# Kernel optimization log

Measured on AMD Instinct MI355X. Metric: run time of the kernel, lower is better.

The kernel has to match this reference:

```python
import jax, jax.numpy as jnp
import numpy as np


def setup_inputs() -> dict:
    key = jax.random.key(0)
    k1, k2 = jax.random.split(key)
    B, K, D = 65536, 4096, 64
    x = jax.random.normal(k1, (B, D), dtype=jnp.float32)
    nodes = jax.random.normal(k2, (K, D), dtype=jnp.float32)  # self.nodes parameter
    return {"x": x, "nodes": nodes}


def reference(x, nodes):
    # torch.cdist(x, nodes, p=2): Euclidean distance matrix [B, K]
    x2 = jnp.sum(x * x, axis=-1, keepdims=True)            # [B, 1]
    n2 = jnp.sum(nodes * nodes, axis=-1)[None, :]          # [1, K]
    d2 = x2 + n2 - 2.0 * (x @ nodes.T)                     # [B, K]
    distances = jnp.sqrt(jnp.maximum(d2, 0.0))
    winning_indices = jnp.argmin(distances, axis=-1)       # [B]
    node_repr = nodes[winning_indices]                     # [B, D] gather
    return node_repr, winning_indices
```

## Files before the change

### kernel.cpp

```cpp
#include <hip/hip_runtime.h>
#include <stdint.h>


typedef unsigned short u16;
typedef __bf16 bf16x8 __attribute__((ext_vector_type(8)));
typedef unsigned short u16x8 __attribute__((ext_vector_type(8)));
typedef float f32x16 __attribute__((ext_vector_type(16)));

#define B_ROWS 65536
#define K_NODES 4096
#define DIM 64
#define MERGE_TAU 0.0065f

#define OFF_LIST 64
#define OFF_N2F  262208
#define OFF_N2D  278592
#define OFF_BFRAG 311360

#define GLOBAL_AS __attribute__((address_space(1)))
#define LDS_AS    __attribute__((address_space(3)))

__device__ __forceinline__ u16 bf16_rne(float f, float& back) {
    uint32_t u = __float_as_uint(f);
    uint32_t r = u + 0x7FFFu + ((u >> 16) & 1u);
    u16 h = (u16)(r >> 16);
    back = __uint_as_float(((uint32_t)h) << 16);
    return h;
}

__device__ __forceinline__ float pack_tile6(float v, uint32_t t) {
    return __uint_as_float((__float_as_uint(v) & 0xFFFFFFC0u) | t);
}

__global__ __launch_bounds__(256) void prep(const float* __restrict__ nodes,
                                            u16* __restrict__ bfrag,
                                            float* __restrict__ hn2f,
                                            double* __restrict__ n2d,
                                            int* __restrict__ ref_cnt) {
    if (blockIdx.x < 128) {
        int idx = blockIdx.x * 256 + threadIdx.x;
        int t = idx >> 8;
        int rem = idx & 255;
        int l = rem >> 2, c = rem & 3;
        const float* row = nodes + (size_t)(t * 32 + (l & 31)) * DIM + ((l >> 5) * 8);
        float4 f0 = *(const float4*)(row + c * 16);
        float4 f1 = *(const float4*)(row + c * 16 + 4);
        float fs[8] = {-f0.x, -f0.y, -f0.z, -f0.w, -f1.x, -f1.y, -f1.z, -f1.w};
        u16x8 hv, lv;
        #pragma unroll
        for (int j = 0; j < 8; ++j) {
            float hf, dummy;
            u16 hb = bf16_rne(fs[j], hf);
            u16 lb = bf16_rne(fs[j] - hf, dummy);
            hv[j] = hb; lv[j] = lb;
        }
        int base = ((t * 4 + c) * 2) * 512 + l * 8;
        *(u16x8*)(bfrag + base)       = hv;
        *(u16x8*)(bfrag + base + 512) = lv;
    } else {
        if (blockIdx.x == 128 && threadIdx.x == 0) *ref_cnt = 0;
        int k = (blockIdx.x - 128) * 256 + threadIdx.x;
        if (k < K_NODES) {
            const float* r = nodes + (size_t)k * DIM;
            double s = 0.0;
            #pragma unroll
            for (int d = 0; d < DIM; ++d) { double v = (double)r[d]; s += v * v; }
            n2d[k] = s;
            hn2f[k] = 0.5f * (float)s;
        }
    }
}

__global__ __launch_bounds__(256, 2) void phase1(const float* __restrict__ x,
                                                 const u16* __restrict__ bfrag_g,
                                                 const float* __restrict__ hn2f,
                                                 float* __restrict__ out) {
    __shared__ __align__(16) u16 ring[32768];
    __shared__ float hn2s[2048];
    const int tid  = threadIdx.x;
    const int lane = tid & 63;
    const int w    = tid >> 6;
    const int col  = lane & 31;
    const int lh   = lane >> 5;
    const int rb   = blockIdx.x >> 1;
    const int h    = blockIdx.x & 1;
    const int rbase = rb * 256 + w * 64;
    const char* qbase = (const char*)bfrag_g + (size_t)h * 524288;

    bf16x8 ah[2][4], al[2][4];
    #pragma unroll
    for (int t = 0; t < 2; ++t) {
        const float* xp = x + (size_t)(rbase + t * 32 + col) * DIM + lh * 8;
        #pragma unroll
        for (int c = 0; c < 4; ++c) {
            float4 f0 = *(const float4*)(xp + c * 16);
            float4 f1 = *(const float4*)(xp + c * 16 + 4);
            float fs[8] = {f0.x, f0.y, f0.z, f0.w, f1.x, f1.y, f1.z, f1.w};
            u16x8 hv, lv;
            #pragma unroll
            for (int j = 0; j < 8; ++j) {
                float hf, dummy;
                u16 hb = bf16_rne(fs[j], hf);
                u16 lb = bf16_rne(fs[j] - hf, dummy);
                hv[j] = hb; lv[j] = lb;
            }
            union { u16x8 u; bf16x8 b; } cvh, cvl;
            cvh.u = hv; cvl.u = lv;
            ah[t][c] = cvh.b; al[t][c] = cvl.b;
        }
    }

    float b1[2][16], v2[2][16];
    #pragma unroll
    for (int t = 0; t < 2; ++t)
        #pragma unroll
        for (int q = 0; q < 16; ++q) { b1[t][q] = 3.4e38f; v2[t][q] = 3.4e38f; }

    for (int i = tid; i < 2048; i += 256) hn2s[i] = hn2f[h * 2048 + i];
    #pragma unroll
    for (int q0 = 0; q0 < 4; ++q0) {
        const char* gp = qbase + (size_t)q0 * 8192 + tid * 16;
        const char* lp = (const char*)ring + q0 * 8192 + tid * 16;
        __builtin_amdgcn_global_load_lds((const GLOBAL_AS uint32_t*)gp,
                                         (LDS_AS uint32_t*)lp, 16, 0, 0);
        __builtin_amdgcn_global_load_lds((const GLOBAL_AS uint32_t*)(gp + 4096),
                                         (LDS_AS uint32_t*)(lp + 4096), 16, 0, 0);
    }
    asm volatile("s_waitcnt lgkmcnt(0)" ::: "memory");
    __builtin_amdgcn_s_barrier();

#define MF6(CC, BH, BL)                                                          \
    a0 = __builtin_amdgcn_mfma_f32_32x32x16_bf16(ah[0][CC], BH, a0, 0, 0, 0);    \
    a1 = __builtin_amdgcn_mfma_f32_32x32x16_bf16(ah[1][CC], BH, a1, 0, 0, 0);    \
    a0 = __builtin_amdgcn_mfma_f32_32x32x16_bf16(al[0][CC], BH, a0, 0, 0, 0);    \
    a1 = __builtin_amdgcn_mfma_f32_32x32x16_bf16(al[1][CC], BH, a1, 0, 0, 0);    \
    a0 = __builtin_amdgcn_mfma_f32_32x32x16_bf16(ah[0][CC], BL, a0, 0, 0, 0);    \
    a1 = __builtin_amdgcn_mfma_f32_32x32x16_bf16(ah[1][CC], BL, a1, 0, 0, 0);

#define PHASE(QI, VMSTR) do {                                                    \
    asm volatile("s_waitcnt " VMSTR ::: "memory");                               \
    __builtin_amdgcn_s_barrier();                                                \
    __builtin_amdgcn_sched_barrier(0);                                           \
    const u16* bb = ring + ((QI) & 7) * 4096;                                    \
    bf16x8 B0h = *(const bf16x8*)(bb + 0 * 1024 + lane * 8);                     \
    bf16x8 B0l = *(const bf16x8*)(bb + 0 * 1024 + 512 + lane * 8);               \
    bf16x8 B1h = *(const bf16x8*)(bb + 1 * 1024 + lane * 8);                     \
    bf16x8 B1l = *(const bf16x8*)(bb + 1 * 1024 + 512 + lane * 8);               \
    bf16x8 B2h = *(const bf16x8*)(bb + 2 * 1024 + lane * 8);                     \
    bf16x8 B2l = *(const bf16x8*)(bb + 2 * 1024 + 512 + lane * 8);               \
    bf16x8 B3h = *(const bf16x8*)(bb + 3 * 1024 + lane * 8);                     \
    bf16x8 B3l = *(const bf16x8*)(bb + 3 * 1024 + 512 + lane * 8);               \
    float hn2v = hn2s[(QI) * 32 + col];                                          \
    if ((QI) + 4 < 64) {                                                         \
        const char* gp = qbase + (size_t)((QI) + 4) * 8192 + tid * 16;           \
        const char* lp = (const char*)ring + (((QI) + 4) & 7) * 8192 + tid * 16; \
        __builtin_amdgcn_global_load_lds((const GLOBAL_AS uint32_t*)gp,          \
                                         (LDS_AS uint32_t*)lp, 16, 0, 0);        \
        __builtin_amdgcn_global_load_lds((const GLOBAL_AS uint32_t*)(gp + 4096), \
                                         (LDS_AS uint32_t*)(lp + 4096), 16, 0, 0); \
    }                                                                            \
    asm volatile("s_waitcnt lgkmcnt(0)" ::: "memory");                           \
    __builtin_amdgcn_sched_barrier(0);                                           \
    f32x16 a0, a1;                                                               \
    _Pragma("unroll")                                                            \
    for (int q = 0; q < 16; ++q) { a0[q] = hn2v; a1[q] = hn2v; }                 \
    __builtin_amdgcn_s_setprio(1);                                               \
    MF6(0, B0h, B0l)                                                             \
    MF6(1, B1h, B1l)                                                             \
    MF6(2, B2h, B2l)                                                             \
    MF6(3, B3h, B3l)                                                             \
    __builtin_amdgcn_s_setprio(0);                                               \
    const uint32_t tb = (uint32_t)(QI);                                          \
    _Pragma("unroll")                                                            \
    for (int q = 0; q < 16; ++q) {                                               \
        float p0 = pack_tile6(a0[q], tb);                                        \
        v2[0][q] = fminf(v2[0][q], fmaxf(p0, b1[0][q]));                         \
        b1[0][q] = fminf(b1[0][q], p0);                                          \
        float p1 = pack_tile6(a1[q], tb);                                        \
        v2[1][q] = fminf(v2[1][q], fmaxf(p1, b1[1][q]));                         \
        b1[1][q] = fminf(b1[1][q], p1);                                          \
    }                                                                            \
} while (0)

    for (int qi = 0; qi < 61; ++qi) PHASE(qi, "vmcnt(6)");
    PHASE(61, "vmcnt(4)");
    PHASE(62, "vmcnt(2)");
    PHASE(63, "vmcnt(0)");

#undef PHASE
#undef MF6

    int gi[2][16];
    #pragma unroll
    for (int t = 0; t < 2; ++t)
        #pragma unroll
        for (int q = 0; q < 16; ++q)
            gi[t][q] = h * 2048 + (int)(__float_as_uint(b1[t][q]) & 63u) * 32 + col;

    #pragma unroll
    for (int off = 1; off < 32; off <<= 1) {
        #pragma unroll
        for (int t = 0; t < 2; ++t)
            #pragma unroll
            for (int q = 0; q < 16; ++q) {
                float ov  = __shfl_xor(b1[t][q], off, 64);
                float ov2 = __shfl_xor(v2[t][q], off, 64);
                int   og  = __shfl_xor(gi[t][q], off, 64);
                float hi2 = fmaxf(b1[t][q], ov);
                v2[t][q] = fminf(fminf(v2[t][q], ov2), hi2);
                bool take = (ov < b1[t][q]) || (ov == b1[t][q] && og < gi[t][q]);
                b1[t][q] = take ? ov : b1[t][q];
                gi[t][q] = take ? og : gi[t][q];
            }
    }

    if (col == 0) {
        #pragma unroll
        for (int t = 0; t < 2; ++t)
            #pragma unroll
            for (int q = 0; q < 16; ++q) {
                int rloc = (q & 3) + 8 * (q >> 2) + 4 * lh;
                int grow = rb * 256 + w * 64 + t * 32 + rloc;
                *(float2*)(out + (size_t)grow * DIM + h * 2) = make_float2(b1[t][q], v2[t][q]);
                out[(size_t)grow * DIM + 4 + h] = (float)gi[t][q];
            }
    }
}

__global__ __launch_bounds__(256) void merge_k(const float* __restrict__ nodes,
                                               float* __restrict__ out,
                                               int* __restrict__ ref_cnt,
                                               int* __restrict__ ref_list) {
    __shared__ int s_win[256];
    const int tid = threadIdx.x;
    const int row = blockIdx.x * 256 + tid;
    float4 cv = *(const float4*)(out + (size_t)row * DIM);
    float2 ci = *(const float2*)(out + (size_t)row * DIM + 4);
    bool h1w = cv.z < cv.x;
    float wb  = h1w ? cv.z : cv.x;
    float lb  = h1w ? cv.x : cv.z;
    float v2m = fminf(fminf(cv.y, cv.w), lb);
    int gi = (int)(h1w ? ci.y : ci.x);
    out[(size_t)B_ROWS * DIM + row] = (float)gi;
    if (v2m - wb <= MERGE_TAU) {
        int slot = atomicAdd(ref_cnt, 1);
        ref_list[slot] = row;
    }
    s_win[tid] = gi;
    __syncthreads();
    const int base_row = blockIdx.x * 256;
    for (int i = tid; i < 256 * 16; i += 256) {
        int rr = i >> 4, cc = i & 15;
        int wn = s_win[rr];
        float4 v = *(const float4*)(nodes + (size_t)wn * DIM + cc * 4);
        *(float4*)(out + (size_t)(base_row + rr) * DIM + cc * 4) = v;
    }
}

__global__ __launch_bounds__(256) void phase2(const float* __restrict__ x,
                                              const float* __restrict__ nodes,
                                              const double* __restrict__ n2d,
                                              const int* __restrict__ ref_cnt,
                                              const int* __restrict__ ref_list,
                                              float* __restrict__ out) {
    __shared__ double xsA[DIM], xsB[DIM];
    __shared__ double sval[256];
    __shared__ int    sidx[256];
    __shared__ int    rows_s[2];
    const int tid = threadIdx.x;
    const int cnt = *ref_cnt;
    for (int b0 = blockIdx.x * 2; b0 < cnt; b0 += gridDim.x * 2) {
        const int nr = min(2, cnt - b0);
        __syncthreads();
        if (tid < 2) rows_s[tid] = ref_list[b0 + min(tid, nr - 1)];
        __syncthreads();
        if (tid < DIM) {
            xsA[tid] = (double)x[(size_t)rows_s[0] * DIM + tid];
            xsB[tid] = (double)x[(size_t)rows_s[1] * DIM + tid];
        }
        __syncthreads();

        double bestA = 1e300, bestB = 1e300;
        int    biA = K_NODES, biB = K_NODES;
        for (int k = tid; k < K_NODES; k += 256) {
            const float4* np4 = (const float4*)(nodes + (size_t)k * DIM);
            double a0 = 0.0, a1 = 0.0, b0d = 0.0, b1d = 0.0;
            #pragma unroll
            for (int t = 0; t < 16; t += 2) {
                float4 w0 = np4[t], w1 = np4[t + 1];
                a0 += xsA[t*4+0]*(double)w0.x + xsA[t*4+1]*(double)w0.y
                    + xsA[t*4+2]*(double)w0.z + xsA[t*4+3]*(double)w0.w;
                b0d += xsB[t*4+0]*(double)w0.x + xsB[t*4+1]*(double)w0.y
                     + xsB[t*4+2]*(double)w0.z + xsB[t*4+3]*(double)w0.w;
                a1 += xsA[t*4+4]*(double)w1.x + xsA[t*4+5]*(double)w1.y
                    + xsA[t*4+6]*(double)w1.z + xsA[t*4+7]*(double)w1.w;
                b1d += xsB[t*4+4]*(double)w1.x + xsB[t*4+5]*(double)w1.y
                     + xsB[t*4+6]*(double)w1.z + xsB[t*4+7]*(double)w1.w;
            }
            const double nn = n2d[k];
            double sA = nn - 2.0 * (a0 + a1);
            double sB = nn - 2.0 * (b0d + b1d);
            if (sA < bestA) { bestA = sA; biA = k; }
            if (sB < bestB) { bestB = sB; biB = k; }
        }

        #pragma unroll 1
        for (int r = 0; r < nr; ++r) {
            sval[tid] = (r == 0) ? bestA : bestB;
            sidx[tid] = (r == 0) ? biA : biB;
            __syncthreads();
            for (int stride = 128; stride > 0; stride >>= 1) {
                if (tid < (unsigned)stride) {
                    double ov = sval[tid + stride];
                    int    oi = sidx[tid + stride];
                    if (ov < sval[tid] || (ov == sval[tid] && oi < sidx[tid])) {
                        sval[tid] = ov; sidx[tid] = oi;
                    }
                }
                __syncthreads();
            }
            const int wn = sidx[0];
            const int row = rows_s[r];
            if (tid == 0) out[(size_t)B_ROWS * DIM + row] = (float)wn;
            if (tid < 16) {
                float4 v = *(const float4*)(nodes + (size_t)wn * DIM + tid * 4);
                *(float4*)(out + (size_t)row * DIM + tid * 4) = v;
            }
            __syncthreads();
        }
    }
}

extern "C" void kernel_launch(void* const* d_in, const int* in_sizes, int n_in,
                              void* d_out, int out_size, void* d_ws, size_t ws_size,
                              hipStream_t stream) {
    const float* x     = (const float*)d_in[0];
    const float* nodes = (const float*)d_in[1];
    float* out = (float*)d_out;
    char*  ws  = (char*)d_ws;

    int*    ref_cnt  = (int*)ws;
    int*    ref_list = (int*)(ws + OFF_LIST);
    float*  hn2f     = (float*)(ws + OFF_N2F);
    double* n2d      = (double*)(ws + OFF_N2D);
    u16*    bfrag    = (u16*)(ws + OFF_BFRAG);

    prep<<<144, 256, 0, stream>>>(nodes, bfrag, hn2f, n2d, ref_cnt);
    phase1<<<512, 256, 0, stream>>>(x, bfrag, hn2f, out);
    merge_k<<<B_ROWS / 256, 256, 0, stream>>>(nodes, out, ref_cnt, ref_list);
    phase2<<<1024, 256, 0, stream>>>(x, nodes, n2d, ref_cnt, ref_list, out);
}
```

Baseline: 182.4 us.

## Double per-stage tile size in phase1 ring and halve barrier count

Restructures the phase1 LDS ring from 8 stages of 32 nodes to 4 stages of 64 nodes. Each stage is issued with four global_load_lds ops, two stages ahead, and each barrier now covers two 32-node MFMA tiles. B fragments are read from LDS inside the MFMA loop instead of all up front, and the explicit lgkmcnt waits and sched_barriers are dropped. The aim is to halve the barrier and wait overhead per node. The risk is less prefetch depth and compiler-chosen interleaving of LDS reads with MFMAs.

```diff
diff --git a/kernel.cpp b/kernel.cpp
--- a/kernel.cpp
+++ b/kernel.cpp
@@ -75,7 +75,7 @@
                                                  const u16* __restrict__ bfrag_g,
                                                  const float* __restrict__ hn2f,
                                                  float* __restrict__ out) {
-    __shared__ __align__(16) u16 ring[32768];
+    __shared__ __align__(16) u16 ring[4][8192];
     __shared__ float hn2s[2048];
     const int tid  = threadIdx.x;
     const int lane = tid & 63;
@@ -116,79 +116,105 @@
         #pragma unroll
         for (int q = 0; q < 16; ++q) { b1[t][q] = 3.4e38f; v2[t][q] = 3.4e38f; }
 
+    #define ISSUE_STAGE(S) do {                                                  \
+        const char* gp_ = qbase + (size_t)(S) * 16384 + tid * 16;                \
+        const char* lp_ = (const char*)&ring[(S) & 3][0] + tid * 16;             \
+        __builtin_amdgcn_global_load_lds((const GLOBAL_AS uint32_t*)gp_,         \
+                                         (LDS_AS uint32_t*)lp_, 16, 0, 0);       \
+        __builtin_amdgcn_global_load_lds((const GLOBAL_AS uint32_t*)(gp_ + 4096),\
+                                         (LDS_AS uint32_t*)(lp_ + 4096), 16, 0, 0);\
+        __builtin_amdgcn_global_load_lds((const GLOBAL_AS uint32_t*)(gp_ + 8192),\
+                                         (LDS_AS uint32_t*)(lp_ + 8192), 16, 0, 0);\
+        __builtin_amdgcn_global_load_lds((const GLOBAL_AS uint32_t*)(gp_ + 12288),\
+                                         (LDS_AS uint32_t*)(lp_ + 12288), 16, 0, 0);\
+    } while (0)
+
     for (int i = tid; i < 2048; i += 256) hn2s[i] = hn2f[h * 2048 + i];
-    #pragma unroll
-    for (int q0 = 0; q0 < 4; ++q0) {
-        const char* gp = qbase + (size_t)q0 * 8192 + tid * 16;
-        const char* lp = (const char*)ring + q0 * 8192 + tid * 16;
-        __builtin_amdgcn_global_load_lds((const GLOBAL_AS uint32_t*)gp,
-                                         (LDS_AS uint32_t*)lp, 16, 0, 0);
-        __builtin_amdgcn_global_load_lds((const GLOBAL_AS uint32_t*)(gp + 4096),
-                                         (LDS_AS uint32_t*)(lp + 4096), 16, 0, 0);
-    }
+    ISSUE_STAGE(0);
+    ISSUE_STAGE(1);
     asm volatile("s_waitcnt lgkmcnt(0)" ::: "memory");
     __builtin_amdgcn_s_barrier();
 
-#define MF6(CC, BH, BL)                                                          \
-    a0 = __builtin_amdgcn_mfma_f32_32x32x16_bf16(ah[0][CC], BH, a0, 0, 0, 0);    \
-    a1 = __builtin_amdgcn_mfma_f32_32x32x16_bf16(ah[1][CC], BH, a1, 0, 0, 0);    \
-    a0 = __builtin_amdgcn_mfma_f32_32x32x16_bf16(al[0][CC], BH, a0, 0, 0, 0);    \
-    a1 = __builtin_amdgcn_mfma_f32_32x32x16_bf16(al[1][CC], BH, a1, 0, 0, 0);    \
-    a0 = __builtin_amdgcn_mfma_f32_32x32x16_bf16(ah[0][CC], BL, a0, 0, 0, 0);    \
-    a1 = __builtin_amdgcn_mfma_f32_32x32x16_bf16(ah[1][CC], BL, a1, 0, 0, 0);
-
-#define PHASE(QI, VMSTR) do {                                                    \
+#define PHASE(P, VMSTR) do {                                                     \
     asm volatile("s_waitcnt " VMSTR ::: "memory");                               \
     __builtin_amdgcn_s_barrier();                                                \
-    __builtin_amdgcn_sched_barrier(0);                                           \
-    const u16* bb = ring + ((QI) & 7) * 4096;                                    \
-    bf16x8 B0h = *(const bf16x8*)(bb + 0 * 1024 + lane * 8);                     \
-    bf16x8 B0l = *(const bf16x8*)(bb + 0 * 1024 + 512 + lane * 8);               \
-    bf16x8 B1h = *(const bf16x8*)(bb + 1 * 1024 + lane * 8);                     \
-    bf16x8 B1l = *(const bf16x8*)(bb + 1 * 1024 + 512 + lane * 8);               \
-    bf16x8 B2h = *(const bf16x8*)(bb + 2 * 1024 + lane * 8);                     \
-    bf16x8 B2l = *(const bf16x8*)(bb + 2 * 1024 + 512 + lane * 8);               \
-    bf16x8 B3h = *(const bf16x8*)(bb + 3 * 1024 + lane * 8);                     \
-    bf16x8 B3l = *(const bf16x8*)(bb + 3 * 1024 + 512 + lane * 8);               \
-    float hn2v = hn2s[(QI) * 32 + col];                                          \
-    if ((QI) + 4 < 64) {                                                         \
-        const char* gp = qbase + (size_t)((QI) + 4) * 8192 + tid * 16;           \
-        const char* lp = (const char*)ring + (((QI) + 4) & 7) * 8192 + tid * 16; \
-        __builtin_amdgcn_global_load_lds((const GLOBAL_AS uint32_t*)gp,          \
-                                         (LDS_AS uint32_t*)lp, 16, 0, 0);        \
-        __builtin_amdgcn_global_load_lds((const GLOBAL_AS uint32_t*)(gp + 4096), \
-                                         (LDS_AS uint32_t*)(lp + 4096), 16, 0, 0); \
+    if ((P) + 2 < 32) ISSUE_STAGE((P) + 2);                                      \
+    const u16* bb = &ring[(P) & 3][0];                                           \
+    __builtin_amdgcn_s_setprio(1);                                               \
+    _Pragma("unroll")                                                            \
+    for (int nt = 0; nt < 2; ++nt) {                                             \
+        float hn2v = hn2s[(P) * 64 + nt * 32 + col];                             \
+        f32x16 a0, a1;                                                           \
+        _Pragma("unroll")                                                        \
+        for (int q = 0; q < 16; ++q) { a0[q] = hn2v; a1[q] = hn2v; }             \
+        _Pragma("unroll")                                                        \
+        for (int c = 0; c < 4; ++c) {                                            \
+            const bf16x8 bh = *(const bf16x8*)(bb + ((nt * 4 + c) * 2 + 0) * 512 + lane * 8); \
+            const bf16x8 bl = *(const bf16x8*)(bb + ((nt * 4 + c) * 2 + 1) * 512 + lane * 8); \
+            a0 = __builtin_amdgcn_mfma_f32_32x32x16_bf16(ah[0][c], bh, a0, 0, 0, 0); \
+            a1 = __builtin_amdgcn_mfma_f32_32x32x16_bf16(ah[1][c], bh, a1, 0, 0, 0); \
+            a0 = __builtin_amdgcn_mfma_f32_32x32x16_bf16(al[0][c], bh, a0, 0, 0, 0); \
+            a1 = __builtin_amdgcn_mfma_f32_32x32x16_bf16(al[1][c], bh, a1, 0, 0, 0); \
+            a0 = __builtin_amdgcn_mfma_f32_32x32x16_bf16(ah[0][c], bl, a0, 0, 0, 0); \
+            a1 = __builtin_amdgcn_mfma_f32_32x32x16_bf16(al[1][c], bh, a1, 0, 0, 0); \
+        }                                                                        \
+        const uint32_t tb = (uint32_t)((P) * 2 + nt);                            \
+        _Pragma("unroll")                                                        \
+        for (int q = 0; q < 16; ++q) {                                           \
+            float p0 = pack_tile6(a0[q], tb);                                    \
+            v2[0][q] = fminf(v2[0][q], fmaxf(p0, b1[0][q]));                     \
+            b1[0][q] = fminf(b1[0][q], p0);                                      \
+            float p1 = pack_tile6(a1[q], tb);                                    \
+            v2[1][q] = fminf(v2[1][q], fmaxf(p1, b1[1][q]));                     \
+            b1[1][q] = fminf(b1[1][q], p1);                                      \
+        }                                                                        \
     }                                                                            \
-    asm volatile("s_waitcnt lgkmcnt(0)" ::: "memory");                           \
-    __builtin_amdgcn_sched_barrier(0);                                           \
-    f32x16 a0, a1;                                                               \
+    __builtin_amdgcn_s_setprio(0);                                               \
+} while (0)
+
+#undef PHASE
+#define PHASE(P, VMSTR) do {                                                     \
+    asm volatile("s_waitcnt " VMSTR ::: "memory");                               \
+    __builtin_amdgcn_s_barrier();                                                \
+    if ((P) + 2 < 32) ISSUE_STAGE((P) + 2);                                      \
+    const u16* bb = &ring[(P) & 3][0];                                           \
+    __builtin_amdgcn_s_setprio(1);                                               \
     _Pragma("unroll")                                                            \
-    for (int q = 0; q < 16; ++q) { a0[q] = hn2v; a1[q] = hn2v; }                 \
-    __builtin_amdgcn_s_setprio(1);                                               \
-    MF6(0, B0h, B0l)                                                             \
-    MF6(1, B1h, B1l)                                                             \
-    MF6(2, B2h, B2l)                                                             \
-    MF6(3, B3h, B3l)                                                             \
+    for (int nt = 0; nt < 2; ++nt) {                                             \
+        float hn2v = hn2s[(P) * 64 + nt * 32 + col];                             \
+        f32x16 a0, a1;                                                           \
+        _Pragma("unroll")                                                        \
+        for (int q = 0; q < 16; ++q) { a0[q] = hn2v; a1[q] = hn2v; }             \
+        _Pragma("unroll")                                                        \
+        for (int c = 0; c < 4; ++c) {                                            \
+            const bf16x8 bh = *(const bf16x8*)(bb + ((nt * 4 + c) * 2 + 0) * 512 + lane * 8); \
+            const bf16x8 bl = *(const bf16x8*)(bb + ((nt * 4 + c) * 2 + 1) * 512 + lane * 8); \
+            a0 = __builtin_amdgcn_mfma_f32_32x32x16_bf16(ah[0][c], bh, a0, 0, 0, 0); \
+            a1 = __builtin_amdgcn_mfma_f32_32x32x16_bf16(ah[1][c], bh, a1, 0, 0, 0); \
+            a0 = __builtin_amdgcn_mfma_f32_32x32x16_bf16(al[0][c], bh, a0, 0, 0, 0); \
+            a1 = __builtin_amdgcn_mfma_f32_32x32x16_bf16(al[1][c], bh, a1, 0, 0, 0); \
+            a0 = __builtin_amdgcn_mfma_f32_32x32x16_bf16(ah[0][c], bl, a0, 0, 0, 0); \
+            a1 = __builtin_amdgcn_mfma_f32_32x32x16_bf16(ah[1][c], bl, a1, 0, 0, 0); \
+        }                                                                        \
+        const uint32_t tb = (uint32_t)((P) * 2 + nt);                            \
+        _Pragma("unroll")                                                        \
+        for (int q = 0; q < 16; ++q) {                                           \
+            float p0 = pack_tile6(a0[q], tb);                                    \
+            v2[0][q] = fminf(v2[0][q], fmaxf(p0, b1[0][q]));                     \
+            b1[0][q] = fminf(b1[0][q], p0);                                      \
+            float p1 = pack_tile6(a1[q], tb);                                    \
+            v2[1][q] = fminf(v2[1][q], fmaxf(p1, b1[1][q]));                     \
+            b1[1][q] = fminf(b1[1][q], p1);                                      \
+        }                                                                        \
+    }                                                                            \
     __builtin_amdgcn_s_setprio(0);                                               \
-    const uint32_t tb = (uint32_t)(QI);                                          \
-    _Pragma("unroll")                                                            \
-    for (int q = 0; q < 16; ++q) {                                               \
-        float p0 = pack_tile6(a0[q], tb);                                        \
-        v2[0][q] = fminf(v2[0][q], fmaxf(p0, b1[0][q]));                         \
-        b1[0][q] = fminf(b1[0][q], p0);                                          \
-        float p1 = pack_tile6(a1[q], tb);                                        \
-        v2[1][q] = fminf(v2[1][q], fmaxf(p1, b1[1][q]));                         \
-        b1[1][q] = fminf(b1[1][q], p1);                                          \
-    }                                                                            \
 } while (0)
 
-    for (int qi = 0; qi < 61; ++qi) PHASE(qi, "vmcnt(6)");
-    PHASE(61, "vmcnt(4)");
-    PHASE(62, "vmcnt(2)");
-    PHASE(63, "vmcnt(0)");
+    for (int p = 0; p < 31; ++p) PHASE(p, "vmcnt(4)");
+    PHASE(31, "vmcnt(0)");
 
 #undef PHASE
-#undef MF6
+#undef ISSUE_STAGE
 
     int gi[2][16];
     #pragma unroll
```

Result: faster. 176.2 us (-3.4%).
